# Performance work log

Measured on AMD Instinct MI355X. Metric: run time of the kernel, lower is better.

## Reference

```python
import jax, jax.numpy as jnp
import numpy as np

V, E, H, ENC2, L_LAYERS = 1024, 512, 1024, 1024, 3
SOS, EOS = 1, 2


def lstm_cell(x, h, c, W_ih, W_hh, b_ih, b_hh):
    # PyTorch LSTMCell: gates ordered i, f, g, o
    gates = x @ W_ih.T + b_ih + h @ W_hh.T + b_hh
    i, f, g, o = jnp.split(gates, 4, axis=-1)
    i = jax.nn.sigmoid(i)
    f = jax.nn.sigmoid(f)
    g = jnp.tanh(g)
    o = jax.nn.sigmoid(o)
    c = f * c + i * g
    h = o * jnp.tanh(c)
    return h, c


def setup_inputs() -> dict:
    key = jax.random.key(0)
    ks = jax.random.split(key, 20)
    s = 0.05
    inp = {
        'tokens': jax.random.randint(ks[0], (16, 256), 0, V),
        'encoder_outputs': jax.random.normal(ks[1], (16, 512, ENC2), jnp.float32),
        'embedding': jax.random.normal(ks[2], (V, E), jnp.float32) * s,
        # layer 0: input = embedding + encoder context
        'W_ih0': jax.random.normal(ks[3], (4 * H, E + ENC2), jnp.float32) * s,
        'W_hh0': jax.random.normal(ks[4], (4 * H, H), jnp.float32) * s,
        'b_ih0': jnp.zeros((4 * H,), jnp.float32),
        'b_hh0': jnp.zeros((4 * H,), jnp.float32),
        'W_ih1': jax.random.normal(ks[5], (4 * H, H), jnp.float32) * s,
        'W_hh1': jax.random.normal(ks[6], (4 * H, H), jnp.float32) * s,
        'b_ih1': jnp.zeros((4 * H,), jnp.float32),
        'b_hh1': jnp.zeros((4 * H,), jnp.float32),
        'W_ih2': jax.random.normal(ks[7], (4 * H, H), jnp.float32) * s,
        'W_hh2': jax.random.normal(ks[8], (4 * H, H), jnp.float32) * s,
        'b_ih2': jnp.zeros((4 * H,), jnp.float32),
        'b_hh2': jnp.zeros((4 * H,), jnp.float32),
        'W1': jax.random.normal(ks[9], (H, ENC2 + H), jnp.float32) * s,
        'b1': jnp.zeros((H,), jnp.float32),
        'W2': jax.random.normal(ks[10], (V, H), jnp.float32) * s,
        'b2': jnp.zeros((V,), jnp.float32),
    }
    return inp


def reference(tokens, encoder_outputs, embedding,
              W_ih0, W_hh0, b_ih0, b_hh0,
              W_ih1, W_hh1, b_ih1, b_hh1,
              W_ih2, W_hh2, b_ih2, b_hh2,
              W1, b1, W2, b2):
    B, L = tokens.shape
    dtype = encoder_outputs.dtype
    # teacher forcing sequences: dec_in = [sos, y], dec_out = [y, eos]
    dec_in = jnp.concatenate([jnp.full((B, 1), SOS, tokens.dtype), tokens], axis=1)   # [B, T]
    dec_out = jnp.concatenate([tokens, jnp.full((B, 1), EOS, tokens.dtype)], axis=1)  # [B, T]
    T = L + 1

    emb = embedding[dec_in]  # [B, T, E]
    # NOTE: the original forward feeds initial_context (zeros) as the LSTM input
    # context at EVERY step (it is never updated), so the recurrence does not
    # depend on attention and can be scanned independently.
    xs = jnp.concatenate([emb, jnp.zeros((B, T, ENC2), dtype)], axis=-1)  # [B, T, E+ENC2]
    xs = jnp.swapaxes(xs, 0, 1)  # time-major [T, B, E+ENC2]

    z = jnp.zeros((B, H), dtype)
    init = (z, z, z, z, z, z)

    def step(carry, x_t):
        h0, c0, h1, c1, h2, c2 = carry
        h0, c0 = lstm_cell(x_t, h0, c0, W_ih0, W_hh0, b_ih0, b_hh0)
        h1, c1 = lstm_cell(h0, h1, c1, W_ih1, W_hh1, b_ih1, b_hh1)
        h2, c2 = lstm_cell(h1, h2, c2, W_ih2, W_hh2, b_ih2, b_hh2)
        return (h0, c0, h1, c1, h2, c2), h2

    _, hs = jax.lax.scan(step, init, xs)      # [T, B, H]
    hs = jnp.swapaxes(hs, 0, 1)               # [B, T, H]

    # dot-product attention over encoder outputs (vectorized over all steps)
    scores = jnp.einsum('bth,bsh->bts', hs, encoder_outputs)   # [B, T, S]
    attn = jax.nn.softmax(scores, axis=-1)
    ctx = jnp.einsum('bts,bsh->bth', attn, encoder_outputs)    # [B, T, ENC2]

    mlp_in = jnp.concatenate([hs, ctx], axis=-1)               # [B, T, H+ENC2]
    hidden = jnp.tanh(mlp_in @ W1.T + b1)
    logits = hidden @ W2.T + b2                                # [B, T, V]

    logp = jax.nn.log_softmax(logits, axis=-1)
    nll = -jnp.take_along_axis(logp, dec_out[..., None], axis=-1)[..., 0]
    return jnp.mean(nll)
```

## Files before the change

kernel.cpp:

```cpp
#include <hip/hip_runtime.h>
#include <math.h>


namespace {
constexpr int TT = 257;
constexpr int BT = 4112;
constexpr int NSTEP = 259;
constexpr int NWG = 256;

constexpr size_t OFF_EMBB = 0;
constexpr size_t OFF_H0H  = 524288;
constexpr size_t OFF_H1H  = 4751360;
constexpr size_t OFF_H2H  = 8978432;
constexpr size_t OFF_ENCB = 0;
constexpr size_t OFF_ENCT = 13205504;
constexpr size_t OFF_W1B  = 21594112;
constexpr size_t OFF_W2B  = 23691264;
constexpr size_t OFF_SC   = 24739840;
constexpr size_t OFF_CTX  = 26845184;
constexpr size_t OFF_HID  = 31055872;
constexpr size_t OFF_LG   = OFF_SC;
constexpr size_t END_BF   = 35266560;
constexpr size_t OFF_INT_BYTES = END_BF * 2;
constexpr int    ARRIVE_I0     = 12352;
constexpr size_t TOTAL_BYTES   = OFF_INT_BYTES + (ARRIVE_I0 + 256 * 32 + 16) * 4;
constexpr unsigned SPIN_CAP    = 1u << 24;
}

typedef __attribute__((ext_vector_type(8))) short bf16x8;
typedef __attribute__((ext_vector_type(4))) float f32x4;

__device__ __forceinline__ float bf2f(ushort u) {
    union { unsigned int v; float f; } x; x.v = ((unsigned int)u) << 16; return x.f;
}
__device__ __forceinline__ ushort f2bf(float f) {
    union { float f; unsigned int v; } x; x.f = f;
    return (ushort)((x.v + 0x7fff + ((x.v >> 16) & 1)) >> 16);
}
__device__ __forceinline__ float sigm(float x) { return 1.f / (1.f + __expf(-x)); }

__global__ void k_fail(float* out) { out[0] = -123456.0f; }

__global__ __launch_bounds__(256) void k_init(const int* __restrict__ tokens,
                                              const float* __restrict__ emb,
                                              ushort* __restrict__ wsb,
                                              float* __restrict__ out)
{
    int i = blockIdx.x * 256 + threadIdx.x;
    int* dec_in  = (int*)((char*)wsb + OFF_INT_BYTES);
    int* dec_out = dec_in + 4112;
    int* hsrow   = dec_in + 8224;
    unsigned* flags = (unsigned*)(dec_in + ARRIVE_I0);
    {
        size_t e = (size_t)i * 8;
        float4 a = *(const float4*)(emb + e);
        float4 b = *(const float4*)(emb + e + 4);
        uint4 o;
        o.x = (unsigned)f2bf(a.x) | ((unsigned)f2bf(a.y) << 16);
        o.y = (unsigned)f2bf(a.z) | ((unsigned)f2bf(a.w) << 16);
        o.z = (unsigned)f2bf(b.x) | ((unsigned)f2bf(b.y) << 16);
        o.w = (unsigned)f2bf(b.z) | ((unsigned)f2bf(b.w) << 16);
        *(uint4*)(wsb + OFF_EMBB + e) = o;
    }
    if (i < 16384) {
        wsb[OFF_H0H + i] = 0; wsb[OFF_H1H + i] = 0; wsb[OFF_H2H + i] = 0;
    }
    if (i < 4112) {
        int t = i >> 4, b = i & 15;
        dec_in[i] = (t == 0) ? 1 : tokens[b * 256 + (t - 1)];
        int bb = i / 257, tt = i % 257;
        dec_out[i] = (tt < 256) ? tokens[bb * 256 + tt] : 2;
        hsrow[i] = (tt + 1) * 16 + bb;
    }
    if (i < 256 * 32 + 16) flags[i] = 0u;
    if (i == 0) out[0] = 0.f;
}

__global__ __launch_bounds__(1024, 4) void k_rec_persist(
    ushort* __restrict__ wsb,
    const float* __restrict__ Whh0, const float* __restrict__ Wih0,
    const float* __restrict__ Wih1, const float* __restrict__ Whh1,
    const float* __restrict__ Wih2, const float* __restrict__ Whh2,
    const float* __restrict__ bih0, const float* __restrict__ bhh0,
    const float* __restrict__ bih1, const float* __restrict__ bhh1,
    const float* __restrict__ bih2, const float* __restrict__ bhh2,
    const int* __restrict__ dec_in, unsigned* __restrict__ arrive)
{
    __shared__ float p[16][16][17];

    int tid = threadIdx.x;
    int u = blockIdx.x;
    int w = tid >> 6, lane = tid & 63, l15 = lane & 15, quad = lane >> 4;

    int cell, g0, gcnt;
    if (w < 4)       { cell = 0; g0 = w * 12; gcnt = 12; }
    else if (w < 10) { int wi = w - 4;  cell = 1;
                       g0 = (wi < 4) ? wi * 11 : 44 + (wi - 4) * 10;
                       gcnt = (wi < 4) ? 11 : 10; }
    else             { int wi = w - 10; cell = 2;
                       g0 = (wi < 4) ? wi * 11 : 44 + (wi - 4) * 10;
                       gcnt = (wi < 4) ? 11 : 10; }

    int gt = l15 >> 2, s4 = l15 & 3;
    size_t wrow = (size_t)(gt * 1024 + u * 4 + s4);

    bf16x8 wreg[12];
    #pragma unroll
    for (int gi = 0; gi < 12; ++gi) {
        if (gi < gcnt) {
            int g = g0 + gi;
            const float* src;
            if (cell == 0)
                src = (g < 32) ? Whh0 + wrow * 1024 + (size_t)g * 32
                               : Wih0 + wrow * 1536 + (size_t)(g - 32) * 32;
            else if (cell == 1)
                src = (g < 32) ? Wih1 + wrow * 1024 + (size_t)g * 32
                               : Whh1 + wrow * 1024 + (size_t)(g - 32) * 32;
            else
                src = (g < 32) ? Wih2 + wrow * 1024 + (size_t)g * 32
                               : Whh2 + wrow * 1024 + (size_t)(g - 32) * 32;
            src += quad * 8;
            float4 a = *(const float4*)src;
            float4 b = *(const float4*)(src + 4);
            bf16x8 v;
            v[0] = (short)f2bf(a.x); v[1] = (short)f2bf(a.y);
            v[2] = (short)f2bf(a.z); v[3] = (short)f2bf(a.w);
            v[4] = (short)f2bf(b.x); v[5] = (short)f2bf(b.y);
            v[6] = (short)f2bf(b.z); v[7] = (short)f2bf(b.w);
            wreg[gi] = v;
        }
    }

    int cellE = tid >> 6;
    int sub = tid & 63, bE = sub & 15, sE = sub >> 4;
    int colE = u * 4 + sE;
    float bsum[4] = {0.f, 0.f, 0.f, 0.f};
    float cst = 0.f;
    ushort* hE = nullptr;
    int wloE = 0, whiE = 0;
    if (tid < 192) {
        const float* biE = (cellE == 0) ? bih0 : (cellE == 1) ? bih1 : bih2;
        const float* bhE = (cellE == 0) ? bhh0 : (cellE == 1) ? bhh1 : bhh2;
        #pragma unroll
        for (int gq = 0; gq < 4; ++gq)
            bsum[gq] = biE[gq * 1024 + colE] + bhE[gq * 1024 + colE];
        hE = wsb + ((cellE == 0) ? OFF_H0H : (cellE == 1) ? OFF_H1H : OFF_H2H);
        wloE = (cellE == 0) ? 0 : (cellE == 1) ? 4 : 10;
        whiE = (cellE == 0) ? 4 : (cellE == 1) ? 10 : 16;
    }

    ushort* h0h = wsb + OFF_H0H;
    ushort* h1h = wsb + OFF_H1H;
    ushort* h2h = wsb + OFF_H2H;
    const ushort* embB = wsb + OFF_EMBB;
    size_t aoff = (size_t)l15 * 1024 + quad * 8;

    for (int d = 0; d < NSTEP; ++d) {
        int t = d - cell;
        f32x4 acc = {0.f, 0.f, 0.f, 0.f};
        if (t >= 0 && t < TT) {
            const ushort* a0p;
            const ushort* a1p;
            if (cell == 0) {
                a0p = h0h + (size_t)t * 16384 + aoff;
                int tok = dec_in[t * 16 + l15];
                a1p = embB + (size_t)tok * 512 + quad * 8;
            } else if (cell == 1) {
                a0p = h0h + (size_t)(t + 1) * 16384 + aoff;
                a1p = h1h + (size_t)t * 16384 + aoff;
            } else {
                a0p = h1h + (size_t)(t + 1) * 16384 + aoff;
                a1p = h2h + (size_t)t * 16384 + aoff;
            }
            #pragma unroll
            for (int gi = 0; gi < 12; ++gi) {
                if (gi < gcnt) {
                    int g = g0 + gi;
                    bf16x8 af = (g < 32)
                        ? *(const bf16x8*)(a0p + (size_t)g * 32)
                        : *(const bf16x8*)(a1p + (size_t)(g - 32) * 32);
                    acc = __builtin_amdgcn_mfma_f32_16x16x32_bf16(
                        af, wreg[gi], acc, 0, 0, 0);
                }
            }
        }
        #pragma unroll
        for (int r = 0; r < 4; ++r) p[w][quad * 4 + r][l15] = acc[r];
        __syncthreads();

        if (tid < 192) {
            int tE = d - cellE;
            if (tE >= 0 && tE < TT) {
                float gv[4];
                #pragma unroll
                for (int gq = 0; gq < 4; ++gq) {
                    float a2 = bsum[gq];
                    for (int ww = wloE; ww < whiE; ++ww)
                        a2 += p[ww][bE][gq * 4 + sE];
                    gv[gq] = a2;
                }
                float ig = sigm(gv[0]), fg = sigm(gv[1]);
                float gg = tanhf(gv[2]), og = sigm(gv[3]);
                cst = fg * cst + ig * gg;
                ushort hus = f2bf(og * tanhf(cst));
                unsigned hi = __shfl_down((unsigned)hus, 16, 64);
                if ((sE & 1) == 0) {
                    unsigned* hp = (unsigned*)(hE + (size_t)(tE + 1) * 16384
                                               + (size_t)bE * 1024 + colE);
                    __hip_atomic_store(hp, (unsigned)hus | (hi << 16),
                                       __ATOMIC_RELAXED, __HIP_MEMORY_SCOPE_AGENT);
                }
            }
        }

        asm volatile("s_waitcnt vmcnt(0)" ::: "memory");
        __syncthreads();
        unsigned stamp = (unsigned)(d + 1);
        if (tid == 0)
            __hip_atomic_store(arrive + u * 32, stamp,
                               __ATOMIC_RELAXED, __HIP_MEMORY_SCOPE_AGENT);
        if (tid < 256) {
            unsigned spins = 0;
            while (__hip_atomic_load(arrive + tid * 32, __ATOMIC_RELAXED,
                                     __HIP_MEMORY_SCOPE_AGENT) < stamp) {
                __builtin_amdgcn_s_sleep(1);
                if (++spins > SPIN_CAP) break;
            }
        }
        __syncthreads();
    }
}

__global__ __launch_bounds__(256) void k_cvt_flat(const float* __restrict__ src,
                                                  ushort* __restrict__ dst)
{
    size_t e = ((size_t)blockIdx.x * 256 + threadIdx.x) * 8;
    float4 a = *(const float4*)(src + e);
    float4 b = *(const float4*)(src + e + 4);
    uint4 o;
    o.x = (unsigned)f2bf(a.x) | ((unsigned)f2bf(a.y) << 16);
    o.y = (unsigned)f2bf(a.z) | ((unsigned)f2bf(a.w) << 16);
    o.z = (unsigned)f2bf(b.x) | ((unsigned)f2bf(b.y) << 16);
    o.w = (unsigned)f2bf(b.z) | ((unsigned)f2bf(b.w) << 16);
    *(uint4*)(dst + e) = o;
}

__global__ __launch_bounds__(256) void k_enc_t(const float* __restrict__ enc,
                                               ushort* __restrict__ encT)
{
    __shared__ float tile[32][33];
    int b = blockIdx.z, s0 = blockIdx.x * 32, h0 = blockIdx.y * 32;
    int tx = threadIdx.x & 31, ty = threadIdx.x >> 5;
    const float* src = enc + (size_t)b * 524288;
    #pragma unroll
    for (int i = 0; i < 4; i++) {
        int s = s0 + ty + i * 8;
        tile[ty + i * 8][tx] = src[(size_t)s * 1024 + h0 + tx];
    }
    __syncthreads();
    ushort* dst = encT + (size_t)b * 524288;
    #pragma unroll
    for (int i = 0; i < 4; i++) {
        int h = h0 + ty + i * 8;
        dst[(size_t)h * 512 + s0 + tx] = f2bf(tile[tx][ty + i * 8]);
    }
}

__global__ __launch_bounds__(256) void k_gemm_bb(
    const ushort* __restrict__ A, int lda, long sA, const int* __restrict__ aIdx,
    const ushort* __restrict__ B, int ldb, long sB,
    ushort* __restrict__ C, int ldc, long sC,
    int M, int K, int accum)
{
    int z = blockIdx.z;
    const ushort* Ab = A + (size_t)z * sA;
    const ushort* Bb = B + (size_t)z * sB;
    ushort* Cb = C + (size_t)z * sC;
    int m0 = blockIdx.y * 64, n0 = blockIdx.x * 64;
    int tid = threadIdx.x, w = tid >> 6, lane = tid & 63;
    int l15 = lane & 15, quad = lane >> 4;
    int am = m0 + w * 16 + l15;
    int ar = (am < M) ? (aIdx ? aIdx[am] : am) : (aIdx ? aIdx[0] : 0);
    const ushort* ap = Ab + (size_t)ar * lda + quad * 8;
    const ushort* bp = Bb + (size_t)(n0 + l15) * ldb + quad * 8;
    f32x4 acc[4] = {{0.f,0.f,0.f,0.f},{0.f,0.f,0.f,0.f},{0.f,0.f,0.f,0.f},{0.f,0.f,0.f,0.f}};
    for (int k0 = 0; k0 < K; k0 += 32) {
        bf16x8 af = *(const bf16x8*)(ap + k0);
        #pragma unroll
        for (int j = 0; j < 4; j++) {
            bf16x8 bfb = *(const bf16x8*)(bp + (size_t)j * 16 * ldb + k0);
            acc[j] = __builtin_amdgcn_mfma_f32_16x16x32_bf16(af, bfb, acc[j], 0, 0, 0);
        }
    }
    #pragma unroll
    for (int j = 0; j < 4; j++)
        #pragma unroll
        for (int r = 0; r < 4; r++) {
            int row = m0 + w * 16 + quad * 4 + r;
            if (row < M) {
                ushort* cp = Cb + (size_t)row * ldc + n0 + j * 16 + l15;
                float v = acc[j][r];
                if (accum) v += bf2f(*cp);
                *cp = f2bf(v);
            }
        }
}

__global__ __launch_bounds__(256) void k_softmax_b(ushort* __restrict__ sc)
{
    __shared__ float red[4];
    ushort* p = sc + (size_t)blockIdx.x * 512;
    int tid = threadIdx.x;
    float a = bf2f(p[tid]), b = bf2f(p[tid + 256]);
    float m = fmaxf(a, b);
    for (int o = 32; o; o >>= 1) m = fmaxf(m, __shfl_xor(m, o, 64));
    if ((tid & 63) == 0) red[tid >> 6] = m;
    __syncthreads();
    m = fmaxf(fmaxf(red[0], red[1]), fmaxf(red[2], red[3]));
    __syncthreads();
    float ea = __expf(a - m), eb = __expf(b - m);
    float s = ea + eb;
    for (int o = 32; o; o >>= 1) s += __shfl_xor(s, o, 64);
    if ((tid & 63) == 0) red[tid >> 6] = s;
    __syncthreads();
    s = red[0] + red[1] + red[2] + red[3];
    float inv = 1.f / s;
    p[tid] = f2bf(ea * inv);
    p[tid + 256] = f2bf(eb * inv);
}

__global__ __launch_bounds__(256) void k_tanh_bias_b(ushort* __restrict__ hid,
                                                     const float* __restrict__ b1)
{
    size_t i = (size_t)blockIdx.x * 256 + threadIdx.x;
    hid[i] = f2bf(tanhf(bf2f(hid[i]) + b1[i & 1023]));
}

__global__ __launch_bounds__(256) void k_loss_b(const ushort* __restrict__ logits,
                                                const float* __restrict__ b2,
                                                const int* __restrict__ dec_out_m,
                                                float* __restrict__ out)
{
    __shared__ float red[4];
    int m = blockIdx.x;
    const ushort* p = logits + (size_t)m * 1024;
    int tid = threadIdx.x;
    float v0 = bf2f(p[tid]) + b2[tid];
    float v1 = bf2f(p[tid + 256]) + b2[tid + 256];
    float v2 = bf2f(p[tid + 512]) + b2[tid + 512];
    float v3 = bf2f(p[tid + 768]) + b2[tid + 768];
    float mx = fmaxf(fmaxf(v0, v1), fmaxf(v2, v3));
    for (int o = 32; o; o >>= 1) mx = fmaxf(mx, __shfl_xor(mx, o, 64));
    if ((tid & 63) == 0) red[tid >> 6] = mx;
    __syncthreads();
    mx = fmaxf(fmaxf(red[0], red[1]), fmaxf(red[2], red[3]));
    __syncthreads();
    float s = __expf(v0 - mx) + __expf(v1 - mx) + __expf(v2 - mx) + __expf(v3 - mx);
    for (int o = 32; o; o >>= 1) s += __shfl_xor(s, o, 64);
    if ((tid & 63) == 0) red[tid >> 6] = s;
    __syncthreads();
    if (tid == 0) {
        float ssum = red[0] + red[1] + red[2] + red[3];
        int tgt = dec_out_m[m];
        float tv = bf2f(p[tgt]) + b2[tgt];
        atomicAdd(out, (mx + logf(ssum) - tv) * (1.0f / 4112.0f));
    }
}

extern "C" void kernel_launch(void* const* d_in, const int* in_sizes, int n_in,
                              void* d_out, int out_size, void* d_ws, size_t ws_size,
                              hipStream_t stream)
{
    const int*   tokens = (const int*)d_in[0];
    const float* enc    = (const float*)d_in[1];
    const float* emb    = (const float*)d_in[2];
    const float* Wih0   = (const float*)d_in[3];
    const float* Whh0   = (const float*)d_in[4];
    const float* bih0   = (const float*)d_in[5];
    const float* bhh0   = (const float*)d_in[6];
    const float* Wih1   = (const float*)d_in[7];
    const float* Whh1   = (const float*)d_in[8];
    const float* bih1   = (const float*)d_in[9];
    const float* bhh1   = (const float*)d_in[10];
    const float* Wih2   = (const float*)d_in[11];
    const float* Whh2   = (const float*)d_in[12];
    const float* bih2   = (const float*)d_in[13];
    const float* bhh2   = (const float*)d_in[14];
    const float* W1     = (const float*)d_in[15];
    const float* b1     = (const float*)d_in[16];
    const float* W2     = (const float*)d_in[17];
    const float* b2     = (const float*)d_in[18];

    float* out = (float*)d_out;
    if (ws_size < TOTAL_BYTES) { k_fail<<<1, 1, 0, stream>>>(out); return; }

    ushort* wsb  = (ushort*)d_ws;
    ushort* h2h  = wsb + OFF_H2H;
    ushort* sc   = wsb + OFF_SC;
    ushort* ctx  = wsb + OFF_CTX;
    ushort* hid  = wsb + OFF_HID;
    ushort* lg   = wsb + OFF_LG;
    ushort* encB = wsb + OFF_ENCB;
    ushort* encT = wsb + OFF_ENCT;
    ushort* W1b  = wsb + OFF_W1B;
    ushort* W2b  = wsb + OFF_W2B;
    int* dec_in  = (int*)((char*)d_ws + OFF_INT_BYTES);
    int* dec_out = dec_in + 4112;
    int* hsrow   = dec_in + 8224;
    unsigned* arrive = (unsigned*)(dec_in + ARRIVE_I0);

    k_init<<<256, 256, 0, stream>>>(tokens, emb, wsb, out);

    k_rec_persist<<<NWG, 1024, 0, stream>>>(wsb, Whh0, Wih0, Wih1, Whh1,
                                            Wih2, Whh2, bih0, bhh0, bih1, bhh1,
                                            bih2, bhh2, dec_in, arrive);

    k_cvt_flat<<<4096, 256, 0, stream>>>(enc, encB);
    k_enc_t<<<dim3(16, 32, 16), 256, 0, stream>>>(enc, encT);
    k_cvt_flat<<<1024, 256, 0, stream>>>(W1, W1b);
    k_cvt_flat<<<512, 256, 0, stream>>>(W2, W2b);

    k_gemm_bb<<<dim3(8, 5, 16), 256, 0, stream>>>(h2h + 16384, 16384, 1024, nullptr,
                                                  encB, 1024, 524288,
                                                  sc, 512, 131584, TT, 1024, 0);
    k_softmax_b<<<4112, 256, 0, stream>>>(sc);
    k_gemm_bb<<<dim3(16, 5, 16), 256, 0, stream>>>(sc, 512, 131584, nullptr,
                                                   encT, 512, 524288,
                                                   ctx, 1024, 263168, TT, 512, 0);
    k_gemm_bb<<<dim3(16, 65, 1), 256, 0, stream>>>(h2h, 1024, 0, hsrow,
                                                   W1b, 2048, 0,
                                                   hid, 1024, 0, BT, 1024, 0);
    k_gemm_bb<<<dim3(16, 65, 1), 256, 0, stream>>>(ctx, 1024, 0, nullptr,
                                                   W1b + 1024, 2048, 0,
                                                   hid, 1024, 0, BT, 1024, 1);
    k_tanh_bias_b<<<16448, 256, 0, stream>>>(hid, b1);
    k_gemm_bb<<<dim3(16, 65, 1), 256, 0, stream>>>(hid, 1024, 0, nullptr,
                                                   W2b, 1024, 0,
                                                   lg, 1024, 0, BT, 1024, 0);
    k_loss_b<<<4112, 256, 0, stream>>>(lg, b2, dec_out, out);
}
```

Baseline: 3.105 ms.

## Replace all-to-all grid barrier with master-gather and go-flag broadcast; prefetch token

The per-step grid barrier changes from every workgroup polling all 256 arrive flags to a centralized scheme. Workgroup 0 gathers the arrivals without sleeping and then publishes a single go stamp, which the other workgroups poll from one thread. This cuts polling traffic on the flag lines and may shorten barrier latency on the serial 259-step recurrence. The layer-0 token index is also loaded one step ahead to take its latency off the critical path, and the spin cap is lowered.

```diff
diff --git a/kernel.cpp b/kernel.cpp
--- a/kernel.cpp
+++ b/kernel.cpp
@@ -23,8 +23,9 @@
 constexpr size_t END_BF   = 35266560;
 constexpr size_t OFF_INT_BYTES = END_BF * 2;
 constexpr int    ARRIVE_I0     = 12352;
-constexpr size_t TOTAL_BYTES   = OFF_INT_BYTES + (ARRIVE_I0 + 256 * 32 + 16) * 4;
-constexpr unsigned SPIN_CAP    = 1u << 24;
+constexpr int    GO_I0         = ARRIVE_I0 + 256 * 32;
+constexpr size_t TOTAL_BYTES   = OFF_INT_BYTES + (GO_I0 + 16) * 4;
+constexpr unsigned SPIN_CAP    = 1u << 22;
 }
 
 typedef __attribute__((ext_vector_type(8))) short bf16x8;
@@ -84,7 +85,8 @@
     const float* __restrict__ bih0, const float* __restrict__ bhh0,
     const float* __restrict__ bih1, const float* __restrict__ bhh1,
     const float* __restrict__ bih2, const float* __restrict__ bhh2,
-    const int* __restrict__ dec_in, unsigned* __restrict__ arrive)
+    const int* __restrict__ dec_in,
+    unsigned* __restrict__ arrive, unsigned* __restrict__ go)
 {
     __shared__ float p[16][16][17];
 
@@ -155,6 +157,9 @@
     const ushort* embB = wsb + OFF_EMBB;
     size_t aoff = (size_t)l15 * 1024 + quad * 8;
 
+    int tokv = 0;
+    if (cell == 0) tokv = dec_in[l15];
+
     for (int d = 0; d < NSTEP; ++d) {
         int t = d - cell;
         f32x4 acc = {0.f, 0.f, 0.f, 0.f};
@@ -163,8 +168,9 @@
             const ushort* a1p;
             if (cell == 0) {
                 a0p = h0h + (size_t)t * 16384 + aoff;
-                int tok = dec_in[t * 16 + l15];
-                a1p = embB + (size_t)tok * 512 + quad * 8;
+                a1p = embB + (size_t)tokv * 512 + quad * 8;
+                int tn = (t + 1 < TT) ? (t + 1) : (TT - 1);
+                tokv = dec_in[tn * 16 + l15];
             } else if (cell == 1) {
                 a0p = h0h + (size_t)(t + 1) * 16384 + aoff;
                 a1p = h1h + (size_t)t * 16384 + aoff;
@@ -216,18 +222,31 @@
         asm volatile("s_waitcnt vmcnt(0)" ::: "memory");
         __syncthreads();
         unsigned stamp = (unsigned)(d + 1);
-        if (tid == 0)
-            __hip_atomic_store(arrive + u * 32, stamp,
-                               __ATOMIC_RELAXED, __HIP_MEMORY_SCOPE_AGENT);
-        if (tid < 256) {
-            unsigned spins = 0;
-            while (__hip_atomic_load(arrive + tid * 32, __ATOMIC_RELAXED,
-                                     __HIP_MEMORY_SCOPE_AGENT) < stamp) {
-                __builtin_amdgcn_s_sleep(1);
-                if (++spins > SPIN_CAP) break;
-            }
-        }
-        __syncthreads();
+        if (u == 0) {
+            if (tid > 0 && tid < 256) {
+                unsigned spins = 0;
+                while (__hip_atomic_load(arrive + tid * 32, __ATOMIC_RELAXED,
+                                         __HIP_MEMORY_SCOPE_AGENT) < stamp) {
+                    if (++spins > SPIN_CAP) break;
+                }
+            }
+            __syncthreads();
+            if (tid == 0)
+                __hip_atomic_store(go, stamp, __ATOMIC_RELAXED,
+                                   __HIP_MEMORY_SCOPE_AGENT);
+        } else {
+            if (tid == 0) {
+                __hip_atomic_store(arrive + u * 32, stamp, __ATOMIC_RELAXED,
+                                   __HIP_MEMORY_SCOPE_AGENT);
+                unsigned spins = 0;
+                while (__hip_atomic_load(go, __ATOMIC_RELAXED,
+                                         __HIP_MEMORY_SCOPE_AGENT) < stamp) {
+                    __builtin_amdgcn_s_sleep(1);
+                    if (++spins > SPIN_CAP) break;
+                }
+            }
+            __syncthreads();
+        }
     }
 }
 
@@ -408,12 +427,13 @@
     int* dec_out = dec_in + 4112;
     int* hsrow   = dec_in + 8224;
     unsigned* arrive = (unsigned*)(dec_in + ARRIVE_I0);
+    unsigned* go     = (unsigned*)(dec_in + GO_I0);
 
     k_init<<<256, 256, 0, stream>>>(tokens, emb, wsb, out);
 
     k_rec_persist<<<NWG, 1024, 0, stream>>>(wsb, Whh0, Wih0, Wih1, Whh1,
                                             Wih2, Whh2, bih0, bhh0, bih1, bhh1,
-                                            bih2, bhh2, dec_in, arrive);
+                                            bih2, bhh2, dec_in, arrive, go);
 
     k_cvt_flat<<<4096, 256, 0, stream>>>(enc, encB);
     k_enc_t<<<dim3(16, 32, 16), 256, 0, stream>>>(enc, encT);
```

Result: no change. 3.083 ms (-0.7%).
